# Kernel tuning notes

Hardware: AMD Instinct MI355X
Metric: run time of the kernel (lower is better)

Reference implementation:

```python
import jax, jax.numpy as jnp
from jax import lax
import numpy as np

IN, UNITS, BB = 64, 50, 128  # input_size, CfC units, backbone_units (ncps defaults)
B, T = 256, 2048


def setup_inputs() -> dict:
    key = jax.random.key(0)
    ks = jax.random.split(key, 12)
    g = lambda k, s: jax.random.normal(k, s, dtype=jnp.float32) * 0.05
    return {
        "x": jax.random.normal(ks[0], (B, T, IN), dtype=jnp.float32),
        "W_bb": g(ks[1], (IN + UNITS, BB)), "b_bb": jnp.zeros((BB,), jnp.float32),
        "W_ff1": g(ks[2], (BB, UNITS)), "b_ff1": jnp.zeros((UNITS,), jnp.float32),
        "W_ff2": g(ks[3], (BB, UNITS)), "b_ff2": jnp.zeros((UNITS,), jnp.float32),
        "W_ta": g(ks[4], (BB, UNITS)), "b_ta": jnp.zeros((UNITS,), jnp.float32),
        "W_tb": g(ks[5], (BB, UNITS)), "b_tb": jnp.zeros((UNITS,), jnp.float32),
        "W_out": g(ks[6], (UNITS, 1)), "b_out": jnp.zeros((1,), jnp.float32),
    }


def lecun_tanh(x):
    return 1.7159 * jnp.tanh(0.666 * x)


def reference(x, W_bb, b_bb, W_ff1, b_ff1, W_ff2, b_ff2, W_ta, b_ta, W_tb, b_tb, W_out, b_out):
    Bb = x.shape[0]

    def step(h, xt):  # xt: [B, IN], h: [B, UNITS]
        z = jnp.concatenate([xt, h], axis=-1)
        bb = lecun_tanh(z @ W_bb + b_bb)                       # backbone, 1 layer
        ff1 = jnp.tanh(bb @ W_ff1 + b_ff1)
        ff2 = jnp.tanh(bb @ W_ff2 + b_ff2)
        # ts = 1.0 per step => t_interp = sigmoid(time_a + time_b)
        t_interp = jax.nn.sigmoid((bb @ W_ta + b_ta) + (bb @ W_tb + b_tb))
        h_new = ff1 * (1.0 - t_interp) + t_interp * ff2
        return h_new, None

    xs = jnp.swapaxes(x, 0, 1)  # [T, B, IN]
    h0 = jnp.zeros((Bb, W_ff1.shape[1]), x.dtype)
    hT, _ = lax.scan(step, h0, xs)  # final hidden state [B, UNITS]
    # original module: self.linear(hn[-1]) -> readout on last batch row
    return hT[-1] @ W_out + b_out  # shape [1]
```

## Files before the change

kernel.cpp:

```cpp
#include <hip/hip_runtime.h>
#include <math.h>

#define IN    64
#define UNITS 50
#define BBU   128
#define BATCH 256
#define TT    2048

__device__ __forceinline__ float dpp_xor1(float v) {
    int r = __builtin_amdgcn_update_dpp(0, __builtin_bit_cast(int, v),
                                        0xB1, 0xF, 0xF, true);
    return __builtin_bit_cast(float, r);
}
__device__ __forceinline__ float dpp_xor2(float v) {
    int r = __builtin_amdgcn_update_dpp(0, __builtin_bit_cast(int, v),
                                        0x4E, 0xF, 0xF, true);
    return __builtin_bit_cast(float, r);
}

__global__ void xproj_kernel(const float* __restrict__ x,
                             const float* __restrict__ W_bb,
                             const float* __restrict__ b_bb,
                             float* __restrict__ xproj) {
    __shared__ float xr[IN];
    const int t = blockIdx.x;
    const int j = threadIdx.x;
    const float* xrow = x + ((size_t)(BATCH - 1) * TT + t) * IN;
    if (j < IN) xr[j] = xrow[j];
    __syncthreads();
    float acc = b_bb[j];
    #pragma unroll
    for (int k = 0; k < IN; ++k) acc = fmaf(xr[k], W_bb[k * BBU + j], acc);
    xproj[t * BBU + j] = acc;
}

__launch_bounds__(256, 1)
__global__ void cfc_seq_kernel(const float* __restrict__ W_bb,
                               const float* __restrict__ W_ff1, const float* __restrict__ b_ff1,
                               const float* __restrict__ W_ff2, const float* __restrict__ b_ff2,
                               const float* __restrict__ W_ta,  const float* __restrict__ b_ta,
                               const float* __restrict__ W_tb,  const float* __restrict__ b_tb,
                               const float* __restrict__ W_out, const float* __restrict__ b_out,
                               const float* __restrict__ xproj,
                               float* __restrict__ out) {
    __shared__ __align__(16) float h_lds[72];
    __shared__ __align__(16) float bb_lds[144];

    const int tid = threadIdx.x;

    const int j1 = tid >> 1;
    const int s1 = tid & 1;
    float wh[32];
    #pragma unroll
    for (int q = 0; q < 32; ++q)
        wh[q] = (q < 25) ? W_bb[(IN + s1 * 25 + q) * BBU + j1] : 0.f;

    const int q2 = tid >> 2;
    const int r2 = tid & 3;
    const int col = (q2 < UNITS) ? q2 : 0;
    const float msk = (q2 < UNITS) ? 1.f : 0.f;
    float w_f1[32], w_f2[32], w_tt[32];
    #pragma unroll
    for (int i = 0; i < 32; ++i) {
        const int row = r2 * 32 + i;
        w_f1[i] = msk * W_ff1[row * UNITS + col];
        w_f2[i] = msk * W_ff2[row * UNITS + col];
        w_tt[i] = msk * (W_ta[row * UNITS + col] + W_tb[row * UNITS + col]);
    }
    float bias2;
    if (r2 == 0)      bias2 = b_ff1[col];
    else if (r2 == 1) bias2 = b_ff2[col];
    else if (r2 == 2) bias2 = b_ta[col] + b_tb[col];
    else              bias2 = 0.f;
    bias2 *= msk;
    const float kact = (r2 == 2) ? 1.4426950409f : 2.8853900818f;
    const float cact = (r2 == 2) ? 1.f : 2.f;

    if (tid < 72) h_lds[tid] = 0.f;

    float xp_cur = xproj[j1];
    float xp_next;
    __syncthreads();

    for (int t = 0; t < TT; ++t) {
        {
            const int tn = (t + 1 < TT) ? (t + 1) : t;
            xp_next = xproj[tn * BBU + j1];
        }

        {
            const float4* h4 = (const float4*)(h_lds + s1 * 36);
            float p0 = (s1 == 0) ? xp_cur : 0.f;
            float p1 = 0.f, p2 = 0.f, p3 = 0.f;
            #pragma unroll
            for (int k = 0; k < 8; ++k) {
                const float4 v = h4[k];
                p0 = fmaf(v.x, wh[4 * k + 0], p0);
                p1 = fmaf(v.y, wh[4 * k + 1], p1);
                p2 = fmaf(v.z, wh[4 * k + 2], p2);
                p3 = fmaf(v.w, wh[4 * k + 3], p3);
            }
            float a1 = (p0 + p1) + (p2 + p3);
            a1 += dpp_xor1(a1);
            const float bbv = 1.7159f *
                (1.f - 2.f * __builtin_amdgcn_rcpf(
                     __builtin_amdgcn_exp2f(1.9216697945f * a1) + 1.f));
            if (s1 == 0) bb_lds[(j1 >> 5) * 36 + (j1 & 31)] = bbv;
        }
        __syncthreads();

        {
            const float4* bq = (const float4*)(bb_lds + r2 * 36);
            float f1a = 0.f, f1b = 0.f;
            float f2a = 0.f, f2b = 0.f;
            float tta = 0.f, ttb = 0.f;
            #pragma unroll
            for (int k = 0; k < 8; ++k) {
                const float4 v = bq[k];
                f1a = fmaf(v.x, w_f1[4 * k + 0], f1a);
                f2a = fmaf(v.x, w_f2[4 * k + 0], f2a);
                tta = fmaf(v.x, w_tt[4 * k + 0], tta);
                f1b = fmaf(v.y, w_f1[4 * k + 1], f1b);
                f2b = fmaf(v.y, w_f2[4 * k + 1], f2b);
                ttb = fmaf(v.y, w_tt[4 * k + 1], ttb);
                f1a = fmaf(v.z, w_f1[4 * k + 2], f1a);
                f2a = fmaf(v.z, w_f2[4 * k + 2], f2a);
                tta = fmaf(v.z, w_tt[4 * k + 2], tta);
                f1b = fmaf(v.w, w_f1[4 * k + 3], f1b);
                f2b = fmaf(v.w, w_f2[4 * k + 3], f2b);
                ttb = fmaf(v.w, w_tt[4 * k + 3], ttb);
            }
            float f1s = f1a + f1b;
            float f2s = f2a + f2b;
            float tts = tta + ttb;
            f1s += dpp_xor1(f1s);  f1s += dpp_xor2(f1s);
            f2s += dpp_xor1(f2s);  f2s += dpp_xor2(f2s);
            tts += dpp_xor1(tts);  tts += dpp_xor2(tts);
            const float sel = (r2 == 0) ? f1s : ((r2 == 1) ? f2s : tts);
            const float a2 = sel + bias2;
            const float val = 1.f - cact * __builtin_amdgcn_rcpf(
                                  __builtin_amdgcn_exp2f(kact * a2) + 1.f);
            const float f2v = dpp_xor1(val);
            const float tiv = dpp_xor2(val);
            if (r2 == 0 && q2 < UNITS) {
                h_lds[q2 + ((q2 >= 25) ? 11 : 0)] = fmaf(tiv, f2v - val, val);
            }
        }
        xp_cur = xp_next;
        __syncthreads();
    }

    if (tid < 64) {
        float v = 0.f;
        if (tid < UNITS)
            v = h_lds[tid + ((tid >= 25) ? 11 : 0)] * W_out[tid];
        #pragma unroll
        for (int off = 1; off < 64; off <<= 1)
            v += __shfl_xor(v, off);
        if (tid == 0) out[0] = v + b_out[0];
    }
}

extern "C" void kernel_launch(void* const* d_in, const int* in_sizes, int n_in,
                              void* d_out, int out_size, void* d_ws, size_t ws_size,
                              hipStream_t stream) {
    const float* x     = (const float*)d_in[0];
    const float* W_bb  = (const float*)d_in[1];
    const float* b_bb  = (const float*)d_in[2];
    const float* W_ff1 = (const float*)d_in[3];
    const float* b_ff1 = (const float*)d_in[4];
    const float* W_ff2 = (const float*)d_in[5];
    const float* b_ff2 = (const float*)d_in[6];
    const float* W_ta  = (const float*)d_in[7];
    const float* b_ta  = (const float*)d_in[8];
    const float* W_tb  = (const float*)d_in[9];
    const float* b_tb  = (const float*)d_in[10];
    const float* W_out = (const float*)d_in[11];
    const float* b_out = (const float*)d_in[12];
    float* out = (float*)d_out;

    float* xproj = (float*)d_ws;

    xproj_kernel<<<TT, BBU, 0, stream>>>(x, W_bb, b_bb, xproj);
    cfc_seq_kernel<<<1, 256, 0, stream>>>(W_bb,
                                          W_ff1, b_ff1, W_ff2, b_ff2,
                                          W_ta, b_ta, W_tb, b_tb,
                                          W_out, b_out, xproj, out);
}
```

Measured before the change: 1.394 ms.

## Double threads in recurrent kernel to halve per-thread dot-product chains

The single-block sequential CfC kernel goes from 256 to 512 threads. The backbone reduction over the hidden state is now split across 4 lanes instead of 2, and the head matmuls across 8 lanes instead of 4, with extra DPP steps (including a half-row mirror) to combine partial sums. Each head lane now evaluates all three activations itself, removing the per-lane selection and the DPP exchange before the state update. The aim is to shorten the serial FMA and LDS-load chain per timestep. In exchange, each block barrier must synchronise eight waves instead of four, and every step adds more reduction instructions.

```diff
diff --git a/kernel.cpp b/kernel.cpp
--- a/kernel.cpp
+++ b/kernel.cpp
@@ -7,15 +7,20 @@
 #define BATCH 256
 #define TT    2048
 
-__device__ __forceinline__ float dpp_xor1(float v) {
+template <int CTRL>
+__device__ __forceinline__ float dpp_mv(float v) {
     int r = __builtin_amdgcn_update_dpp(0, __builtin_bit_cast(int, v),
-                                        0xB1, 0xF, 0xF, true);
+                                        CTRL, 0xF, 0xF, true);
     return __builtin_bit_cast(float, r);
 }
-__device__ __forceinline__ float dpp_xor2(float v) {
-    int r = __builtin_amdgcn_update_dpp(0, __builtin_bit_cast(int, v),
-                                        0x4E, 0xF, 0xF, true);
-    return __builtin_bit_cast(float, r);
+
+__device__ __forceinline__ float tanh_fast(float x) {
+    return 1.f - 2.f * __builtin_amdgcn_rcpf(
+                    __builtin_amdgcn_exp2f(2.8853900818f * x) + 1.f);
+}
+__device__ __forceinline__ float sigm_fast(float x) {
+    return 1.f - __builtin_amdgcn_rcpf(
+                    __builtin_amdgcn_exp2f(1.4426950409f * x) + 1.f);
 }
 
 __global__ void xproj_kernel(const float* __restrict__ x,
@@ -34,7 +39,7 @@
     xproj[t * BBU + j] = acc;
 }
 
-__launch_bounds__(256, 1)
+__launch_bounds__(512, 2)
 __global__ void cfc_seq_kernel(const float* __restrict__ W_bb,
                                const float* __restrict__ W_ff1, const float* __restrict__ b_ff1,
                                const float* __restrict__ W_ff2, const float* __restrict__ b_ff2,
@@ -43,40 +48,39 @@
                                const float* __restrict__ W_out, const float* __restrict__ b_out,
                                const float* __restrict__ xproj,
                                float* __restrict__ out) {
-    __shared__ __align__(16) float h_lds[72];
-    __shared__ __align__(16) float bb_lds[144];
+    __shared__ __align__(16) float h_lds[80];
+    __shared__ __align__(16) float bb_lds[160];
 
     const int tid = threadIdx.x;
 
-    const int j1 = tid >> 1;
-    const int s1 = tid & 1;
-    float wh[32];
+    const int j1 = tid >> 2;
+    const int s1 = tid & 3;
+    float wh[16];
     #pragma unroll
-    for (int q = 0; q < 32; ++q)
-        wh[q] = (q < 25) ? W_bb[(IN + s1 * 25 + q) * BBU + j1] : 0.f;
+    for (int q = 0; q < 16; ++q) {
+        const int u = s1 * 13 + q;
+        wh[q] = (q < 13 && u < UNITS) ? W_bb[(IN + u) * BBU + j1] : 0.f;
+    }
+    const int bbslot = 20 * (j1 >> 4) + (j1 & 15);
 
-    const int q2 = tid >> 2;
-    const int r2 = tid & 3;
-    const int col = (q2 < UNITS) ? q2 : 0;
-    const float msk = (q2 < UNITS) ? 1.f : 0.f;
-    float w_f1[32], w_f2[32], w_tt[32];
+    const int o2 = tid >> 3;
+    const int g2 = tid & 7;
+    const int col = (o2 < UNITS) ? o2 : 0;
+    const float msk = (o2 < UNITS) ? 1.f : 0.f;
+    float w_f1[16], w_f2[16], w_tt[16];
     #pragma unroll
-    for (int i = 0; i < 32; ++i) {
-        const int row = r2 * 32 + i;
+    for (int i = 0; i < 16; ++i) {
+        const int row = g2 * 16 + i;
         w_f1[i] = msk * W_ff1[row * UNITS + col];
         w_f2[i] = msk * W_ff2[row * UNITS + col];
         w_tt[i] = msk * (W_ta[row * UNITS + col] + W_tb[row * UNITS + col]);
     }
-    float bias2;
-    if (r2 == 0)      bias2 = b_ff1[col];
-    else if (r2 == 1) bias2 = b_ff2[col];
-    else if (r2 == 2) bias2 = b_ta[col] + b_tb[col];
-    else              bias2 = 0.f;
-    bias2 *= msk;
-    const float kact = (r2 == 2) ? 1.4426950409f : 2.8853900818f;
-    const float cact = (r2 == 2) ? 1.f : 2.f;
+    const float bi_f1 = b_ff1[col];
+    const float bi_f2 = b_ff2[col];
+    const float bi_tt = b_ta[col] + b_tb[col];
+    const int hslot = 20 * (col / 13) + (col % 13);
 
-    if (tid < 72) h_lds[tid] = 0.f;
+    if (tid < 80) h_lds[tid] = 0.f;
 
     float xp_cur = xproj[j1];
     float xp_next;
@@ -89,11 +93,11 @@
         }
 
         {
-            const float4* h4 = (const float4*)(h_lds + s1 * 36);
+            const float4* h4 = (const float4*)(h_lds + s1 * 20);
             float p0 = (s1 == 0) ? xp_cur : 0.f;
             float p1 = 0.f, p2 = 0.f, p3 = 0.f;
             #pragma unroll
-            for (int k = 0; k < 8; ++k) {
+            for (int k = 0; k < 4; ++k) {
                 const float4 v = h4[k];
                 p0 = fmaf(v.x, wh[4 * k + 0], p0);
                 p1 = fmaf(v.y, wh[4 * k + 1], p1);
@@ -101,22 +105,22 @@
                 p3 = fmaf(v.w, wh[4 * k + 3], p3);
             }
             float a1 = (p0 + p1) + (p2 + p3);
-            a1 += dpp_xor1(a1);
+            a1 += dpp_mv<0xB1>(a1);
+            a1 += dpp_mv<0x4E>(a1);
             const float bbv = 1.7159f *
                 (1.f - 2.f * __builtin_amdgcn_rcpf(
                      __builtin_amdgcn_exp2f(1.9216697945f * a1) + 1.f));
-            if (s1 == 0) bb_lds[(j1 >> 5) * 36 + (j1 & 31)] = bbv;
+            if (s1 == 0) bb_lds[bbslot] = bbv;
         }
         __syncthreads();
 
         {
-            const float4* bq = (const float4*)(bb_lds + r2 * 36);
-            float f1a = 0.f, f1b = 0.f;
-            float f2a = 0.f, f2b = 0.f;
-            float tta = 0.f, ttb = 0.f;
+            const float4* b4 = (const float4*)(bb_lds + g2 * 20);
+            float f1a = 0.f, f2a = 0.f, tta = 0.f;
+            float f1b = 0.f, f2b = 0.f, ttb = 0.f;
             #pragma unroll
-            for (int k = 0; k < 8; ++k) {
-                const float4 v = bq[k];
+            for (int k = 0; k < 4; ++k) {
+                const float4 v = b4[k];
                 f1a = fmaf(v.x, w_f1[4 * k + 0], f1a);
                 f2a = fmaf(v.x, w_f2[4 * k + 0], f2a);
                 tta = fmaf(v.x, w_tt[4 * k + 0], tta);
@@ -130,20 +134,17 @@
                 f2b = fmaf(v.w, w_f2[4 * k + 3], f2b);
                 ttb = fmaf(v.w, w_tt[4 * k + 3], ttb);
             }
-            float f1s = f1a + f1b;
-            float f2s = f2a + f2b;
-            float tts = tta + ttb;
-            f1s += dpp_xor1(f1s);  f1s += dpp_xor2(f1s);
-            f2s += dpp_xor1(f2s);  f2s += dpp_xor2(f2s);
-            tts += dpp_xor1(tts);  tts += dpp_xor2(tts);
-            const float sel = (r2 == 0) ? f1s : ((r2 == 1) ? f2s : tts);
-            const float a2 = sel + bias2;
-            const float val = 1.f - cact * __builtin_amdgcn_rcpf(
-                                  __builtin_amdgcn_exp2f(kact * a2) + 1.f);
-            const float f2v = dpp_xor1(val);
-            const float tiv = dpp_xor2(val);
-            if (r2 == 0 && q2 < UNITS) {
-                h_lds[q2 + ((q2 >= 25) ? 11 : 0)] = fmaf(tiv, f2v - val, val);
+            float sf1 = f1a + f1b;
+            float sf2 = f2a + f2b;
+            float stt = tta + ttb;
+            sf1 += dpp_mv<0xB1>(sf1); sf1 += dpp_mv<0x4E>(sf1); sf1 += dpp_mv<0x141>(sf1);
+            sf2 += dpp_mv<0xB1>(sf2); sf2 += dpp_mv<0x4E>(sf2); sf2 += dpp_mv<0x141>(sf2);
+            stt += dpp_mv<0xB1>(stt); stt += dpp_mv<0x4E>(stt); stt += dpp_mv<0x141>(stt);
+            const float v1 = tanh_fast(sf1 + bi_f1);
+            const float v2 = tanh_fast(sf2 + bi_f2);
+            const float ti = sigm_fast(stt + bi_tt);
+            if (g2 == 0 && o2 < UNITS) {
+                h_lds[hslot] = fmaf(ti, v2 - v1, v1);
             }
         }
         xp_cur = xp_next;
@@ -153,7 +154,7 @@
     if (tid < 64) {
         float v = 0.f;
         if (tid < UNITS)
-            v = h_lds[tid + ((tid >= 25) ? 11 : 0)] * W_out[tid];
+            v = h_lds[20 * (tid / 13) + (tid % 13)] * W_out[tid];
         #pragma unroll
         for (int off = 1; off < 64; off <<= 1)
             v += __shfl_xor(v, off);
@@ -182,7 +183,7 @@
     float* xproj = (float*)d_ws;
 
     xproj_kernel<<<TT, BBU, 0, stream>>>(x, W_bb, b_bb, xproj);
-    cfc_seq_kernel<<<1, 256, 0, stream>>>(W_bb,
+    cfc_seq_kernel<<<1, 512, 0, stream>>>(W_bb,
                                           W_ff1, b_ff1, W_ff2, b_ff2,
                                           W_ta, b_ta, W_tb, b_tb,
                                           W_out, b_out, xproj, out);
```

After: 1.311 ms. -6.0%, faster.
